# Kernel optimization log

Measured on AMD Instinct MI355X. Metric: run time of the kernel, lower is better.

The kernel has to match this reference:

```python
import jax, jax.numpy as jnp
import numpy as np

EPS = 1e-8

def setup_inputs() -> dict:
    key = jax.random.key(0)
    k0, k1, k2, k3, k4 = jax.random.split(key, 5)
    B, N, K, Q, L, F = 8, 5, 5, 4, 128, 768
    support_emb = jax.random.normal(k0, (B, N, K, L, F), dtype=jnp.float32)
    query_emb = jax.random.normal(k1, (B, N * Q, L, F), dtype=jnp.float32)
    B_mask = jax.random.randint(k2, (B, N, K, L), 0, 2, dtype=jnp.int32)
    I_mask = jax.random.randint(k3, (B, N, K, L), 0, 2, dtype=jnp.int32)
    trigger_label = jax.random.randint(k4, (B, N * Q, L), 0, 2 * N + 1, dtype=jnp.int32)
    return {"support_emb": support_emb, "query_emb": query_emb, "B_mask": B_mask,
            "I_mask": I_mask, "trigger_label": trigger_label, "N": N, "K": K, "Q": Q}

def _proto(support_emb, Bm, Im, N):
    # support_emb: (B,N,K,L,F); Bm/Im: (B,N,K,L) float
    sum_B = jnp.einsum('bnklf,bnkl->bnf', support_emb, Bm)
    cnt_B = Bm.sum((2, 3))[..., None] + EPS
    pB = sum_B / cnt_B                                   # (B,N,F)
    sum_I = jnp.einsum('bnklf,bnkl->bnf', support_emb, Im)
    cnt_I = Im.sum((2, 3))[..., None] + EPS
    pI = sum_I / cnt_I                                   # (B,N,F)
    Om = 1.0 - Bm - Im                                   # (B,N,K,L)
    sum_O = jnp.einsum('bnklf,bnkl->bf', support_emb, Om)
    cnt_O = Om.sum((1, 2, 3))[:, None] + EPS
    pO = sum_O / cnt_O                                   # (B,F)
    Bsz, F = pO.shape
    # interleave: tags [O, B_0, I_0, B_1, I_1, ...]
    pBI = jnp.stack([pB, pI], axis=2).reshape(Bsz, 2 * N, F)
    return jnp.concatenate([pO[:, None, :], pBI], axis=1)  # (B, 2N+1, F)

def reference(support_emb, query_emb, B_mask, I_mask, trigger_label, N, K, Q):
    dt = support_emb.dtype
    Bm = B_mask.astype(dt)
    Im = I_mask.astype(dt)
    prototype = _proto(support_emb, Bm, Im, N)             # (B, 2N+1, F)
    # similarity: broadcast dot product -> batched GEMM
    logits = jnp.einsum('bqlf,btf->bqlt', query_emb, prototype)  # (B, NQ, L, 2N+1)
    T = logits.shape[-1]
    flat = logits.reshape(-1, T)
    pred = jnp.argmax(flat, axis=1)
    lab = trigger_label.reshape(-1)
    logp = jax.nn.log_softmax(flat, axis=-1)
    loss = -jnp.take_along_axis(logp, lab[:, None], axis=1).mean()
    return (loss, logits, pred)
```

## Files before the change

kernel.cpp:

```cpp
#include <hip/hip_runtime.h>
#include <cstdint>
#include <cstddef>

#define EPS 1e-8f

#define Bsz 8
#define Nn  5
#define Kk  5
#define Ll  128
#define Ff  768
#define Tt  11
#define KL  640
#define ROWS_PER_B 2560
#define NROWS 20480
#define F4  192
#define BN  40

#define S1_ROWS 16
#define S1_CH   (KL / S1_ROWS)
#define S1_NBLK (BN * S1_CH)
#define PART_STRIDE (3 * Ff)
#define PART_STRIDE4 (PART_STRIDE / 4)

typedef float v2f __attribute__((ext_vector_type(2)));

__global__ __launch_bounds__(192) void stage1(
    const float* __restrict__ sup,
    const int*   __restrict__ Bm,
    const int*   __restrict__ Im,
    float* __restrict__ part,
    float* __restrict__ pcnt)
{
    int blk = blockIdx.x;
    int bn  = blk / S1_CH;
    int ch  = blk - bn * S1_CH;
    int tid = threadIdx.x;

    const float4* sp = (const float4*)(sup + ((size_t)bn * KL + ch * S1_ROWS) * Ff) + tid;
    const int*    bp = Bm + bn * KL + ch * S1_ROWS;
    const int*    ip = Im + bn * KL + ch * S1_ROWS;

    v2f tB0 = {0.f,0.f}, tB1 = tB0, tI0 = tB0, tI1 = tB0, tA0 = tB0, tA1 = tB0;
    int cB = 0, cI = 0;

    #pragma unroll
    for (int h = 0; h < 2; ++h) {
        float4 v[8];
        #pragma unroll
        for (int j = 0; j < 8; ++j) v[j] = sp[(h * 8 + j) * F4];
        #pragma unroll
        for (int j = 0; j < 8; ++j) {
            int p = h * 8 + j;
            v2f lo = {v[j].x, v[j].y};
            v2f hi = {v[j].z, v[j].w};
            tA0 += lo; tA1 += hi;
            if (bp[p]) { tB0 += lo; tB1 += hi; ++cB; }
            if (ip[p]) { tI0 += lo; tI1 += hi; ++cI; }
        }
    }

    float4* o = (float4*)(part + (size_t)blk * PART_STRIDE);
    float4 rB = {tB0.x, tB0.y, tB1.x, tB1.y};
    float4 rI = {tI0.x, tI0.y, tI1.x, tI1.y};
    float4 rA = {tA0.x, tA0.y, tA1.x, tA1.y};
    o[tid]          = rB;
    o[F4 + tid]     = rI;
    o[2 * F4 + tid] = rA;

    if (tid == 0) {
        pcnt[2 * (size_t)blk]     = (float)cB;
        pcnt[2 * (size_t)blk + 1] = (float)cI;
    }
}

__global__ __launch_bounds__(256) void stage2(
    const float* __restrict__ part,
    float* __restrict__ bnsum,
    float* __restrict__ loss_out)
{
    int gid = blockIdx.x * 256 + threadIdx.x;
    if (gid == 0) loss_out[0] = 0.0f;

    int bn  = gid / (3 * F4);
    int r   = gid - bn * (3 * F4);
    int set = r / F4;
    int f4  = r - set * F4;

    const float4* src = (const float4*)(part + (size_t)bn * S1_CH * PART_STRIDE + set * Ff) + f4;
    float4 s = {0, 0, 0, 0};
    #pragma unroll
    for (int c8 = 0; c8 < S1_CH / 8; ++c8) {
        float4 v[8];
        #pragma unroll
        for (int j = 0; j < 8; ++j) v[j] = src[(size_t)(c8 * 8 + j) * PART_STRIDE4];
        #pragma unroll
        for (int j = 0; j < 8; ++j) {
            s.x += v[j].x; s.y += v[j].y; s.z += v[j].z; s.w += v[j].w;
        }
    }
    ((float4*)bnsum)[((size_t)bn * 3 + set) * F4 + f4] = s;
}

#define S3_ROWS 64
#define S3_NBLK (NROWS / S3_ROWS)
#define BLKS_PER_B (ROWS_PER_B / S3_ROWS)

__global__ __launch_bounds__(128) void stage3(
    const float* __restrict__ query,
    const float* __restrict__ bnsum,
    const float* __restrict__ pcnt,
    const int*   __restrict__ label,
    float* __restrict__ out_logits,
    float* __restrict__ out_pred,
    float* __restrict__ loss_out)
{
    __shared__ float4 ldsP[Tt * 4 * 49];
    __shared__ float  sCnt[2 * Nn];
    __shared__ float  sScale[Tt];

    int blk = blockIdx.x;
    int b   = blk / BLKS_PER_B;
    int tid = threadIdx.x;

    if (tid < 2 * Nn) sCnt[tid] = 0.0f;
    __syncthreads();
    for (int i = tid; i < 400; i += 128) {
        float v = pcnt[400 * b + i];
        int n   = i / 80;
        int set = i & 1;
        atomicAdd(&sCnt[2 * n + set], v);
    }
    __syncthreads();
    if (tid < Tt) {
        if (tid == 0) {
            float cO = (float)(KL * Nn);
            #pragma unroll
            for (int k = 0; k < 2 * Nn; ++k) cO -= sCnt[k];
            sScale[0] = 1.0f / (cO + EPS);
        } else {
            sScale[tid] = 1.0f / (sCnt[tid - 1] + EPS);
        }
    }
    __syncthreads();

    const float4* bs = (const float4*)bnsum + (size_t)b * Nn * 3 * F4;
    for (int idx = tid; idx < Tt * F4; idx += 128) {
        int t  = idx / F4;
        int f4 = idx - t * F4;
        float4 val;
        if (t == 0) {
            float sx = 0, sy = 0, sz = 0, sw = 0;
            #pragma unroll
            for (int n = 0; n < Nn; ++n) {
                float4 A = bs[(n * 3 + 2) * F4 + f4];
                float4 Bv = bs[(n * 3 + 0) * F4 + f4];
                float4 Iv = bs[(n * 3 + 1) * F4 + f4];
                sx += A.x - Bv.x - Iv.x; sy += A.y - Bv.y - Iv.y;
                sz += A.z - Bv.z - Iv.z; sw += A.w - Bv.w - Iv.w;
            }
            val.x = sx; val.y = sy; val.z = sz; val.w = sw;
        } else {
            int n   = (t - 1) >> 1;
            int set = (t - 1) & 1;
            val = bs[(n * 3 + set) * F4 + f4];
        }
        float sc = sScale[t];
        val.x *= sc; val.y *= sc; val.z *= sc; val.w *= sc;
        int s = f4 / 48, j = f4 - 48 * s;
        ldsP[(t * 4 + s) * 49 + j] = val;
    }
    __syncthreads();

    int w    = tid >> 6;
    int lane = tid & 63;
    int p    = lane >> 2;
    int s    = lane & 3;

    size_t row0 = (size_t)blk * S3_ROWS + w * 32 + p * 2;
    const float4* q0 = (const float4*)(query + row0 * Ff) + s * 48;
    const float4* q1 = q0 + F4;

    float a0[Tt], a1[Tt];
    #pragma unroll
    for (int t = 0; t < Tt; ++t) { a0[t] = 0.0f; a1[t] = 0.0f; }

    const float4* pb = &ldsP[s * 49];
    #pragma unroll 2
    for (int j = 0; j < 48; ++j) {
        float4 u = q0[j];
        float4 v = q1[j];
        #pragma unroll
        for (int t = 0; t < Tt; ++t) {
            float4 pv = pb[t * (4 * 49) + j];
            float d0 = a0[t], d1 = a1[t];
            d0 = fmaf(u.x, pv.x, d0); d0 = fmaf(u.y, pv.y, d0);
            d0 = fmaf(u.z, pv.z, d0); d0 = fmaf(u.w, pv.w, d0);
            d1 = fmaf(v.x, pv.x, d1); d1 = fmaf(v.y, pv.y, d1);
            d1 = fmaf(v.z, pv.z, d1); d1 = fmaf(v.w, pv.w, d1);
            a0[t] = d0; a1[t] = d1;
        }
    }

    #pragma unroll
    for (int t = 0; t < Tt; ++t) {
        a0[t] += __shfl_xor(a0[t], 1, 64); a0[t] += __shfl_xor(a0[t], 2, 64);
        a1[t] += __shfl_xor(a1[t], 1, 64); a1[t] += __shfl_xor(a1[t], 2, 64);
    }

    float wloss = 0.0f;
    if (s == 0) {
        #pragma unroll
        for (int rr = 0; rr < 2; ++rr) {
            size_t grow = row0 + rr;
            float* a = rr ? a1 : a0;
            float m = a[0]; int bt = 0;
            #pragma unroll
            for (int t = 1; t < Tt; ++t) if (a[t] > m) { m = a[t]; bt = t; }
            float sum = 0.0f;
            #pragma unroll
            for (int t = 0; t < Tt; ++t) sum += __expf(a[t] - m);
            int lab = label[grow];
            float labv = a[0];
            #pragma unroll
            for (int t = 1; t < Tt; ++t) labv = (lab == t) ? a[t] : labv;
            #pragma unroll
            for (int t = 0; t < Tt; ++t) out_logits[grow * Tt + t] = a[t];
            out_pred[grow] = (float)bt;
            wloss += (m + __logf(sum)) - labv;
        }
    }
    #pragma unroll
    for (int off = 32; off > 0; off >>= 1) wloss += __shfl_xor(wloss, off, 64);
    if (lane == 0) atomicAdd(loss_out, wloss * (1.0f / (float)NROWS));
}

extern "C" void kernel_launch(void* const* d_in, const int* in_sizes, int n_in,
                              void* d_out, int out_size, void* d_ws, size_t ws_size,
                              hipStream_t stream) {
    const float* sup   = (const float*)d_in[0];
    const float* query = (const float*)d_in[1];
    const int*   Bm    = (const int*)d_in[2];
    const int*   Im    = (const int*)d_in[3];
    const int*   lab   = (const int*)d_in[4];

    float* w     = (float*)d_ws;
    float* part  = w;
    float* pcnt  = part + (size_t)S1_NBLK * PART_STRIDE;
    float* bnsum = pcnt + 2 * S1_NBLK;

    float* loss_out   = (float*)d_out;
    float* out_logits = (float*)d_out + 1;
    float* out_pred   = (float*)d_out + 1 + (size_t)NROWS * Tt;

    stage1<<<S1_NBLK, 192, 0, stream>>>(sup, Bm, Im, part, pcnt);
    stage2<<<90, 256, 0, stream>>>(part, bnsum, loss_out);
    stage3<<<S3_NBLK, 128, 0, stream>>>(query, bnsum, pcnt, lab,
                                        out_logits, out_pred, loss_out);
}
```

Baseline: 201.6 us.

## Split stage3 dot products across 8 lanes per row and batch stage1 loads

Stage3 now assigns one query row per group of 8 lanes, each handling a 24-float4 slice, instead of two rows per 4 lanes. Blocks grow to 256 threads and each block covers 32 rows, and the prototype LDS layout is repadded to match. The aim is more memory-level parallelism and lower register pressure in the dominant query-streaming GEMV. Stage1 now loads all 16 rows and the mask values up front to get more loads in flight. In exchange, each row needs an extra shuffle-reduction step, and there are twice as many blocks, each redoing the prototype LDS setup.

```diff
diff --git a/kernel.cpp b/kernel.cpp
--- a/kernel.cpp
+++ b/kernel.cpp
@@ -40,23 +40,24 @@
     const int*    bp = Bm + bn * KL + ch * S1_ROWS;
     const int*    ip = Im + bn * KL + ch * S1_ROWS;
 
+    float4 v[S1_ROWS];
+    #pragma unroll
+    for (int p = 0; p < S1_ROWS; ++p) v[p] = sp[p * F4];
+
+    int mb[S1_ROWS], mi[S1_ROWS];
+    #pragma unroll
+    for (int p = 0; p < S1_ROWS; ++p) { mb[p] = bp[p]; mi[p] = ip[p]; }
+
     v2f tB0 = {0.f,0.f}, tB1 = tB0, tI0 = tB0, tI1 = tB0, tA0 = tB0, tA1 = tB0;
     int cB = 0, cI = 0;
 
     #pragma unroll
-    for (int h = 0; h < 2; ++h) {
-        float4 v[8];
-        #pragma unroll
-        for (int j = 0; j < 8; ++j) v[j] = sp[(h * 8 + j) * F4];
-        #pragma unroll
-        for (int j = 0; j < 8; ++j) {
-            int p = h * 8 + j;
-            v2f lo = {v[j].x, v[j].y};
-            v2f hi = {v[j].z, v[j].w};
-            tA0 += lo; tA1 += hi;
-            if (bp[p]) { tB0 += lo; tB1 += hi; ++cB; }
-            if (ip[p]) { tI0 += lo; tI1 += hi; ++cI; }
-        }
+    for (int p = 0; p < S1_ROWS; ++p) {
+        v2f lo = {v[p].x, v[p].y};
+        v2f hi = {v[p].z, v[p].w};
+        tA0 += lo; tA1 += hi;
+        if (mb[p]) { tB0 += lo; tB1 += hi; ++cB; }
+        if (mi[p]) { tI0 += lo; tI1 += hi; ++cI; }
     }
 
     float4* o = (float4*)(part + (size_t)blk * PART_STRIDE);
@@ -101,11 +102,14 @@
     ((float4*)bnsum)[((size_t)bn * 3 + set) * F4 + f4] = s;
 }
 
-#define S3_ROWS 64
+#define S3_ROWS 32
 #define S3_NBLK (NROWS / S3_ROWS)
 #define BLKS_PER_B (ROWS_PER_B / S3_ROWS)
-
-__global__ __launch_bounds__(128) void stage3(
+#define SL  8
+#define SW  24
+#define LDS_T (SL * (SW + 1))
+
+__global__ __launch_bounds__(256) void stage3(
     const float* __restrict__ query,
     const float* __restrict__ bnsum,
     const float* __restrict__ pcnt,
@@ -114,7 +118,7 @@
     float* __restrict__ out_pred,
     float* __restrict__ loss_out)
 {
-    __shared__ float4 ldsP[Tt * 4 * 49];
+    __shared__ float4 ldsP[Tt * LDS_T];
     __shared__ float  sCnt[2 * Nn];
     __shared__ float  sScale[Tt];
 
@@ -124,7 +128,7 @@
 
     if (tid < 2 * Nn) sCnt[tid] = 0.0f;
     __syncthreads();
-    for (int i = tid; i < 400; i += 128) {
+    for (int i = tid; i < 400; i += 256) {
         float v = pcnt[400 * b + i];
         int n   = i / 80;
         int set = i & 1;
@@ -144,7 +148,7 @@
     __syncthreads();
 
     const float4* bs = (const float4*)bnsum + (size_t)b * Nn * 3 * F4;
-    for (int idx = tid; idx < Tt * F4; idx += 128) {
+    for (int idx = tid; idx < Tt * F4; idx += 256) {
         int t  = idx / F4;
         int f4 = idx - t * F4;
         float4 val;
@@ -152,7 +156,7 @@
             float sx = 0, sy = 0, sz = 0, sw = 0;
             #pragma unroll
             for (int n = 0; n < Nn; ++n) {
-                float4 A = bs[(n * 3 + 2) * F4 + f4];
+                float4 A  = bs[(n * 3 + 2) * F4 + f4];
                 float4 Bv = bs[(n * 3 + 0) * F4 + f4];
                 float4 Iv = bs[(n * 3 + 1) * F4 + f4];
                 sx += A.x - Bv.x - Iv.x; sy += A.y - Bv.y - Iv.y;
@@ -166,68 +170,67 @@
         }
         float sc = sScale[t];
         val.x *= sc; val.y *= sc; val.z *= sc; val.w *= sc;
-        int s = f4 / 48, j = f4 - 48 * s;
-        ldsP[(t * 4 + s) * 49 + j] = val;
+        int s = f4 / SW, j = f4 - SW * s;
+        ldsP[t * LDS_T + s * (SW + 1) + j] = val;
     }
     __syncthreads();
 
     int w    = tid >> 6;
     int lane = tid & 63;
-    int p    = lane >> 2;
-    int s    = lane & 3;
-
-    size_t row0 = (size_t)blk * S3_ROWS + w * 32 + p * 2;
-    const float4* q0 = (const float4*)(query + row0 * Ff) + s * 48;
-    const float4* q1 = q0 + F4;
-
-    float a0[Tt], a1[Tt];
-    #pragma unroll
-    for (int t = 0; t < Tt; ++t) { a0[t] = 0.0f; a1[t] = 0.0f; }
-
-    const float4* pb = &ldsP[s * 49];
-    #pragma unroll 2
-    for (int j = 0; j < 48; ++j) {
-        float4 u = q0[j];
-        float4 v = q1[j];
-        #pragma unroll
-        for (int t = 0; t < Tt; ++t) {
-            float4 pv = pb[t * (4 * 49) + j];
-            float d0 = a0[t], d1 = a1[t];
-            d0 = fmaf(u.x, pv.x, d0); d0 = fmaf(u.y, pv.y, d0);
-            d0 = fmaf(u.z, pv.z, d0); d0 = fmaf(u.w, pv.w, d0);
-            d1 = fmaf(v.x, pv.x, d1); d1 = fmaf(v.y, pv.y, d1);
-            d1 = fmaf(v.z, pv.z, d1); d1 = fmaf(v.w, pv.w, d1);
-            a0[t] = d0; a1[t] = d1;
+    int p    = lane >> 3;
+    int s    = lane & 7;
+
+    size_t row = (size_t)blk * S3_ROWS + w * 8 + p;
+    const float4* q = (const float4*)(query + row * Ff) + s * SW;
+
+    float acc[Tt];
+    #pragma unroll
+    for (int t = 0; t < Tt; ++t) acc[t] = 0.0f;
+
+    const float4* pb = &ldsP[s * (SW + 1)];
+    #pragma unroll
+    for (int h = 0; h < 2; ++h) {
+        float4 qv[12];
+        #pragma unroll
+        for (int j = 0; j < 12; ++j) qv[j] = q[h * 12 + j];
+        #pragma unroll
+        for (int j = 0; j < 12; ++j) {
+            float4 u = qv[j];
+            int jj = h * 12 + j;
+            #pragma unroll
+            for (int t = 0; t < Tt; ++t) {
+                float4 pv = pb[t * LDS_T + jj];
+                float d = acc[t];
+                d = fmaf(u.x, pv.x, d); d = fmaf(u.y, pv.y, d);
+                d = fmaf(u.z, pv.z, d); d = fmaf(u.w, pv.w, d);
+                acc[t] = d;
+            }
         }
     }
 
     #pragma unroll
     for (int t = 0; t < Tt; ++t) {
-        a0[t] += __shfl_xor(a0[t], 1, 64); a0[t] += __shfl_xor(a0[t], 2, 64);
-        a1[t] += __shfl_xor(a1[t], 1, 64); a1[t] += __shfl_xor(a1[t], 2, 64);
+        acc[t] += __shfl_xor(acc[t], 1, 64);
+        acc[t] += __shfl_xor(acc[t], 2, 64);
+        acc[t] += __shfl_xor(acc[t], 4, 64);
     }
 
     float wloss = 0.0f;
     if (s == 0) {
-        #pragma unroll
-        for (int rr = 0; rr < 2; ++rr) {
-            size_t grow = row0 + rr;
-            float* a = rr ? a1 : a0;
-            float m = a[0]; int bt = 0;
-            #pragma unroll
-            for (int t = 1; t < Tt; ++t) if (a[t] > m) { m = a[t]; bt = t; }
-            float sum = 0.0f;
-            #pragma unroll
-            for (int t = 0; t < Tt; ++t) sum += __expf(a[t] - m);
-            int lab = label[grow];
-            float labv = a[0];
-            #pragma unroll
-            for (int t = 1; t < Tt; ++t) labv = (lab == t) ? a[t] : labv;
-            #pragma unroll
-            for (int t = 0; t < Tt; ++t) out_logits[grow * Tt + t] = a[t];
-            out_pred[grow] = (float)bt;
-            wloss += (m + __logf(sum)) - labv;
-        }
+        float m = acc[0]; int bt = 0;
+        #pragma unroll
+        for (int t = 1; t < Tt; ++t) if (acc[t] > m) { m = acc[t]; bt = t; }
+        float sum = 0.0f;
+        #pragma unroll
+        for (int t = 0; t < Tt; ++t) sum += __expf(acc[t] - m);
+        int lab = label[row];
+        float labv = acc[0];
+        #pragma unroll
+        for (int t = 1; t < Tt; ++t) labv = (lab == t) ? acc[t] : labv;
+        #pragma unroll
+        for (int t = 0; t < Tt; ++t) out_logits[row * Tt + t] = acc[t];
+        out_pred[row] = (float)bt;
+        wloss = (m + __logf(sum)) - labv;
     }
     #pragma unroll
     for (int off = 32; off > 0; off >>= 1) wloss += __shfl_xor(wloss, off, 64);
@@ -254,6 +257,6 @@
 
     stage1<<<S1_NBLK, 192, 0, stream>>>(sup, Bm, Im, part, pcnt);
     stage2<<<90, 256, 0, stream>>>(part, bnsum, loss_out);
-    stage3<<<S3_NBLK, 128, 0, stream>>>(query, bnsum, pcnt, lab,
+    stage3<<<S3_NBLK, 256, 0, stream>>>(query, bnsum, pcnt, lab,
                                         out_logits, out_pred, loss_out);
 }
```

Measured after the change: 212.9 us. 1.06x slower.
